# Kernel optimization log

Measured on AMD Instinct MI355X. Metric: run time of the kernel, lower is better.

## Reference

```python
import jax, jax.numpy as jnp
import numpy as np

# Lens/CCD constants from the source module
DX = 0.00859375
F = 8.0
OX = 5.5 / 2.0   # CCD_width / 2
OY = 7.7 / 2.0   # CCD_length / 2

B, C, H, W = 4, 3, 1024, 2048


def _make_bn(h, w):
    # bn[i, j] = floor((cos(atan(dx*(j-ox)/f)) - 1) * (i - oy)), as in __init__
    j = np.arange(w, dtype=np.float64)
    i = np.arange(h, dtype=np.float64)
    a0 = np.arctan(DX * (j - OX) / F)
    bn = np.floor((np.cos(a0)[None, :] - 1.0) * (i[:, None] - OY))
    return bn.astype(np.int32)


def setup_inputs() -> dict:
    key = jax.random.key(0)
    k1, k2 = jax.random.split(key)
    x = jax.random.normal(k1, (B, C, H, W), dtype=jnp.float32)
    # Conv2d(3, 3, kernel_size=3, bias=False) weight: (out_c, in_c, kh, kw)
    weight = jax.random.normal(k2, (3, 3, 3, 3), dtype=jnp.float32) * 0.1
    bn = jnp.asarray(_make_bn(H, W))  # int32 distortion LUT, shape (H, W)
    return {"x": x, "weight": weight, "bn": bn}


def reference(x, weight, bn):
    B_, C_, H_, W_ = x.shape
    Hi, Wj = H_ - 2, W_ // 2 - 2  # active region: i+2 < H and j+2 < W//2
    i = jnp.arange(Hi)
    j = jnp.arange(Wj)
    p = jnp.arange(3)  # k // 3 (patch row)
    q = jnp.arange(3)  # k % 3  (patch col)
    # column used for the LUT wraps for j >= 256 (j1 = j % 256)
    j1 = jnp.where(j >= 256, j % 256, j)
    rows = i[:, None] + p[None, :]        # (Hi, 3)
    cols = j1[:, None] + q[None, :]       # (Wj, 3)
    # tb(i, j, p, q) = i + p + bn[i + p, j1 + q]
    bn_sel = bn[rows[:, None, :, None], cols[None, :, None, :]]  # (Hi, Wj, 3, 3)
    R = rows[:, None, :, None] + bn_sel                          # source row indices
    # Faithful quirk from the source: patch column index into input is q (0..2),
    # NOT j + q: matrix1[:, :, p, q] = input[:, :, tb, q]
    gathered = x[:, :, R, q]  # (B, C, Hi, Wj, 3, 3)
    out_act = jnp.einsum('bcijpq,ocpq->boij', gathered, weight)  # per-pixel 3x3 conv
    # guard from the source: only write when i + 2 + bn[i+2, j+2] < H
    mask = (i[:, None] + 2 + bn[i[:, None] + 2, j[None, :] + 2]) < H_
    out_act = out_act * mask.astype(out_act.dtype)
    return jnp.zeros((B_, C_, H_, W_), x.dtype).at[:, :, :Hi, :Wj].set(out_act)
```

## Files before the change

### kernel.cpp

```cpp
#include <hip/hip_runtime.h>


#define HH 1024
#define WW 2048
#define HI 1022
#define WJ 1022

typedef float f32x4 __attribute__((ext_vector_type(4)));

__global__ __launch_bounds__(256) void dis_conv_kernel(
    const float* __restrict__ x,
    const float* __restrict__ w,
    const int*   __restrict__ bn,
    float*       __restrict__ out)
{
    const int bi = blockIdx.x;
    const int b  = bi >> 10;
    const int i  = bi & 1023;
    const int t  = threadIdx.x;

    __shared__ __align__(16) float v[3][256];
    __shared__ __align__(16) float mask_s[1024];

    const bool activeRow = (i < HI);

    float acc0 = 0.f, acc1 = 0.f, acc2 = 0.f;
    if (activeRow) {
        int Rv[3][3];
        #pragma unroll
        for (int p = 0; p < 3; ++p) {
            const int* bnrow = bn + (size_t)(i + p) * WW;
            #pragma unroll
            for (int q = 0; q < 3; ++q) {
                int rv = i + p + bnrow[t + q];
                if (rv < 0) rv += HH;
                Rv[p][q] = rv;
            }
        }
        #pragma unroll
        for (int c = 0; c < 3; ++c) {
            const float* xbase = x + (size_t)(b * 3 + c) * (HH * WW);
            #pragma unroll
            for (int p = 0; p < 3; ++p) {
                #pragma unroll
                for (int q = 0; q < 3; ++q) {
                    const float xv = xbase[(size_t)Rv[p][q] * WW + q];
                    acc0 += xv * w[(0 * 3 + c) * 9 + p * 3 + q];
                    acc1 += xv * w[(1 * 3 + c) * 9 + p * 3 + q];
                    acc2 += xv * w[(2 * 3 + c) * 9 + p * 3 + q];
                }
            }
        }
    }
    v[0][t] = acc0;
    v[1][t] = acc1;
    v[2][t] = acc2;

    #pragma unroll
    for (int k = 0; k < 4; ++k) {
        const int j = t + 256 * k;
        float m = 0.f;
        if (activeRow && j < WJ)
            m = ((i + 2) + bn[(size_t)(i + 2) * WW + (j + 2)] < HH) ? 1.f : 0.f;
        mask_s[j] = m;
    }
    __syncthreads();

    const int j4 = t * 4;
    const f32x4 z = (f32x4)(0.f);
    const f32x4 mm = *(const f32x4*)&mask_s[j4];
    #pragma unroll
    for (int o = 0; o < 3; ++o) {
        float* orow = out + (((size_t)(b * 3 + o)) * HH + i) * WW;
        const f32x4 vv = *(const f32x4*)&v[o][j4 & 255];
        const f32x4 rv = vv * mm;
        __builtin_nontemporal_store(rv, (f32x4*)&orow[j4]);
        __builtin_nontemporal_store(z,  (f32x4*)&orow[j4 + 1024]);
    }
}

extern "C" void kernel_launch(void* const* d_in, const int* in_sizes, int n_in,
                              void* d_out, int out_size, void* d_ws, size_t ws_size,
                              hipStream_t stream) {
    const float* x   = (const float*)d_in[0];
    const float* w   = (const float*)d_in[1];
    const int*   bn  = (const int*)d_in[2];
    float*       out = (float*)d_out;

    dis_conv_kernel<<<dim3(4096), dim3(256), 0, stream>>>(x, w, bn, out);
}
```

Baseline: 175.5 us.

## Stage bn rows and x window in LDS, gather from shared memory

Each block now loads the three bn rows it needs and a 64-row window of the first four columns of x for all channels into shared memory with vectorized loads. The per-thread 3x3 gather then reads from LDS, with a fallback to global loads when a source row falls outside the window. The mask is computed from the staged bn row instead of separate scattered global reads. This adds an extra barrier and LDS traffic in exchange for fewer uncoalesced global gathers. The output store pass is unchanged.

```diff
diff --git a/kernel.cpp b/kernel.cpp
--- a/kernel.cpp
+++ b/kernel.cpp
@@ -5,8 +5,10 @@
 #define WW 2048
 #define HI 1022
 #define WJ 1022
+#define XSPAN 64
 
 typedef float f32x4 __attribute__((ext_vector_type(4)));
+typedef int   i32x4 __attribute__((ext_vector_type(4)));
 
 __global__ __launch_bounds__(256) void dis_conv_kernel(
     const float* __restrict__ x,
@@ -20,34 +22,74 @@
     const int t  = threadIdx.x;
 
     __shared__ __align__(16) float v[3][256];
-    __shared__ __align__(16) float mask_s[1024];
+    __shared__ __align__(16) float xs[3][XSPAN][4];
+    __shared__ __align__(16) int   bn01[2][260];
+    __shared__ __align__(16) int   bn2[1024];
 
     const bool activeRow = (i < HI);
+    const int  lo        = (i > 61) ? (i - 61) : 0;
+
+    if (activeRow) {
+        ((i32x4*)bn2)[t] = ((const i32x4*)(bn + (size_t)(i + 2) * WW))[t];
+        if (t < 130) {
+            const int p = (t >= 65) ? 1 : 0;
+            const int k = t - p * 65;
+            ((i32x4*)&bn01[p][0])[k] =
+                ((const i32x4*)(bn + (size_t)(i + p) * WW))[k];
+        }
+        if (t < 192) {
+            const int c = t >> 6;
+            const int r = lo + (t & 63);
+            *(f32x4*)&xs[c][t & 63][0] =
+                *(const f32x4*)(x + ((size_t)(b * 3 + c) * HH + r) * WW);
+        }
+    }
+    __syncthreads();
 
     float acc0 = 0.f, acc1 = 0.f, acc2 = 0.f;
     if (activeRow) {
-        int Rv[3][3];
+        int  rv9[3][3];
+        bool ok = true;
         #pragma unroll
         for (int p = 0; p < 3; ++p) {
-            const int* bnrow = bn + (size_t)(i + p) * WW;
             #pragma unroll
             for (int q = 0; q < 3; ++q) {
-                int rv = i + p + bnrow[t + q];
-                if (rv < 0) rv += HH;
-                Rv[p][q] = rv;
+                const int bv = (p < 2) ? bn01[p][t + q] : bn2[t + q];
+                const int rv = i + p + bv;
+                rv9[p][q] = rv;
+                ok &= ((unsigned)(rv - lo) < XSPAN);
             }
         }
-        #pragma unroll
-        for (int c = 0; c < 3; ++c) {
-            const float* xbase = x + (size_t)(b * 3 + c) * (HH * WW);
+        if (__builtin_expect(ok, 1)) {
             #pragma unroll
-            for (int p = 0; p < 3; ++p) {
+            for (int c = 0; c < 3; ++c) {
                 #pragma unroll
-                for (int q = 0; q < 3; ++q) {
-                    const float xv = xbase[(size_t)Rv[p][q] * WW + q];
-                    acc0 += xv * w[(0 * 3 + c) * 9 + p * 3 + q];
-                    acc1 += xv * w[(1 * 3 + c) * 9 + p * 3 + q];
-                    acc2 += xv * w[(2 * 3 + c) * 9 + p * 3 + q];
+                for (int p = 0; p < 3; ++p) {
+                    #pragma unroll
+                    for (int q = 0; q < 3; ++q) {
+                        const float xv = xs[c][rv9[p][q] - lo][q];
+                        acc0 += xv * w[(0 * 3 + c) * 9 + p * 3 + q];
+                        acc1 += xv * w[(1 * 3 + c) * 9 + p * 3 + q];
+                        acc2 += xv * w[(2 * 3 + c) * 9 + p * 3 + q];
+                    }
+                }
+            }
+        } else {
+            #pragma unroll
+            for (int c = 0; c < 3; ++c) {
+                const float* xbase = x + (size_t)(b * 3 + c) * (HH * WW);
+                #pragma unroll
+                for (int p = 0; p < 3; ++p) {
+                    #pragma unroll
+                    for (int q = 0; q < 3; ++q) {
+                        int rv = rv9[p][q];
+                        if (rv < 0)    rv += HH;
+                        if (rv >= HH)  rv -= HH;
+                        const float xv = xbase[(size_t)rv * WW + q];
+                        acc0 += xv * w[(0 * 3 + c) * 9 + p * 3 + q];
+                        acc1 += xv * w[(1 * 3 + c) * 9 + p * 3 + q];
+                        acc2 += xv * w[(2 * 3 + c) * 9 + p * 3 + q];
+                    }
                 }
             }
         }
@@ -55,20 +97,18 @@
     v[0][t] = acc0;
     v[1][t] = acc1;
     v[2][t] = acc2;
-
-    #pragma unroll
-    for (int k = 0; k < 4; ++k) {
-        const int j = t + 256 * k;
-        float m = 0.f;
-        if (activeRow && j < WJ)
-            m = ((i + 2) + bn[(size_t)(i + 2) * WW + (j + 2)] < HH) ? 1.f : 0.f;
-        mask_s[j] = m;
-    }
     __syncthreads();
 
-    const int j4 = t * 4;
-    const f32x4 z = (f32x4)(0.f);
-    const f32x4 mm = *(const f32x4*)&mask_s[j4];
+    const int   j4 = t * 4;
+    const f32x4 z  = (f32x4)(0.f);
+    f32x4 mm = z;
+    if (activeRow) {
+        #pragma unroll
+        for (int k = 0; k < 4; ++k) {
+            const int j = j4 + k;
+            mm[k] = (j < WJ && (i + 2) + bn2[j + 2] < HH) ? 1.f : 0.f;
+        }
+    }
     #pragma unroll
     for (int o = 0; o < 3; ++o) {
         float* orow = out + (((size_t)(b * 3 + o)) * HH + i) * WW;
```

New measurement: 164.1 us (median of 2 runs). 1.07x faster.
